# Kernel tuning notes

Measured on AMD Instinct MI355X. Metric: run time of the kernel, lower is better.

## Reference

```python
import jax, jax.numpy as jnp
import numpy as np


def setup_inputs() -> dict:
    key = jax.random.key(0)
    k1, k2 = jax.random.split(key)
    B, H, W, C = 16, 768, 1024, 4
    source = jax.random.normal(k1, (B, H, W, C), dtype=jnp.float32)
    # flow in pixels; scale so some warps land out of bounds (exercises safe path)
    flow = jax.random.normal(k2, (B, H, W, 2), dtype=jnp.float32) * 20.0
    return {"source": source, "flow": flow}


def _bilinear_resample_safe(data, warp_x, warp_y):
    """Bilinear sampling of data [B,H,W,C] at (warp_x, warp_y) [B,H,W].
    Out-of-bounds corner taps contribute 0 (TF safe_gather_nd semantics)."""
    B, H, W, C = data.shape
    fx = jnp.floor(warp_x)
    fy = jnp.floor(warp_y)
    w_right = warp_x - fx          # [B,H,W]
    w_down = warp_y - fy
    w_left = 1.0 - w_right
    w_up = 1.0 - w_down
    x0 = fx.astype(jnp.int32)
    y0 = fy.astype(jnp.int32)
    x1 = jnp.ceil(warp_x).astype(jnp.int32)
    y1 = jnp.ceil(warp_y).astype(jnp.int32)
    b = jnp.broadcast_to(jnp.arange(B, dtype=jnp.int32)[:, None, None], warp_x.shape)

    def gather(yy, xx):
        valid = (yy >= 0) & (yy <= H - 1) & (xx >= 0) & (xx <= W - 1)
        yc = jnp.clip(yy, 0, H - 1)
        xc = jnp.clip(xx, 0, W - 1)
        return data[b, yc, xc] * valid[..., None].astype(data.dtype)  # [B,H,W,C]

    wl = w_left[..., None]
    wr = w_right[..., None]
    wu = w_up[..., None]
    wd = w_down[..., None]
    return ((gather(y0, x0) * wl + gather(y0, x1) * wr) * wu
            + (gather(y1, x0) * wl + gather(y1, x1) * wr) * wd)


def reference(source, flow):
    B, H, W, _ = flow.shape
    # flow_to_warp: grid (i=y, j=x) + flow
    gy, gx = jnp.meshgrid(jnp.linspace(0.0, H - 1.0, H),
                          jnp.linspace(0.0, W - 1.0, W), indexing='ij')
    warp = jnp.stack([gy, gx], axis=-1).astype(flow.dtype) + flow  # [B,H,W,2] (y,x)
    warp_y = warp[..., 0]
    warp_x = warp[..., 1]  # resample reverses last dim: (y,x) -> (x,y) for resampler
    warped = _bilinear_resample_safe(source, warp_x, warp_y)
    # mask_invalid on warp coords
    mask = ((warp_y >= 0.0) & (warp_y <= H - 1.0)
            & (warp_x >= 0.0) & (warp_x <= W - 1.0)).astype(warped.dtype)[..., None]
    return warped * mask
```

## Files before the change

### kernel.cpp

```cpp
#include <hip/hip_runtime.h>


typedef float v2f __attribute__((ext_vector_type(2)));
typedef float v4f __attribute__((ext_vector_type(4)));

constexpr int B = 16, H = 768, W = 1024;
constexpr int TX = 64;
constexpr int TY = 16;
constexpr int RPT = 4;
constexpr int XT = W / TX;
constexpr int YT = H / TY;
constexpr int NWG = B * XT * YT;
constexpr int NXCD = 8;
constexpr int CHUNK = NWG / NXCD;

__global__ __launch_bounds__(256) void warp_bilinear_kernel(
    const float* __restrict__ src,
    const float* __restrict__ flow,
    float* __restrict__ out)
{
    unsigned orig = blockIdx.x;
    unsigned t = (orig & (NXCD - 1)) * CHUNK + (orig >> 3);

    int xt = t & (XT - 1);
    unsigned tt = t >> 4;
    int yt = (int)(tt % YT);
    int b  = (int)(tt / YT);

    int tx = threadIdx.x & 63;
    int wv = threadIdx.x >> 6;

    int x     = (xt << 6) + tx;
    int ybase = yt * TY + wv * RPT;

    const float4* sb = (const float4*)src + b * (H * W);
    const v2f*    fb = (const v2f*)flow;
    v4f*          ob = (v4f*)out;

    float xf = (float)x;

#pragma unroll
    for (int r = 0; r < RPT; ++r) {
        int y   = ybase + r;
        int pix = (b * H + y) * W + x;

        v2f fl = __builtin_nontemporal_load(fb + pix);
        float wy = (float)y + fl.x;
        float wx = xf       + fl.y;

        v4f result = {0.f, 0.f, 0.f, 0.f};

        bool valid = (wy >= 0.f) & (wy <= (float)(H - 1)) &
                     (wx >= 0.f) & (wx <= (float)(W - 1));
        if (valid) {
            float fx = floorf(wx);
            float fy = floorf(wy);
            int x0 = (int)fx;
            int y0 = (int)fy;
            int x1 = (int)ceilf(wx);
            int y1 = (int)ceilf(wy);
            float wr = wx - fx;
            float wd = wy - fy;
            float wl = 1.f - wr;
            float wu = 1.f - wd;

            const float4* row0 = sb + y0 * W;
            const float4* row1 = sb + y1 * W;
            float4 g00 = row0[x0];
            float4 g01 = row0[x1];
            float4 g10 = row1[x0];
            float4 g11 = row1[x1];

            result.x = (g00.x * wl + g01.x * wr) * wu + (g10.x * wl + g11.x * wr) * wd;
            result.y = (g00.y * wl + g01.y * wr) * wu + (g10.y * wl + g11.y * wr) * wd;
            result.z = (g00.z * wl + g01.z * wr) * wu + (g10.z * wl + g11.z * wr) * wd;
            result.w = (g00.w * wl + g01.w * wr) * wu + (g10.w * wl + g11.w * wr) * wd;
        }

        __builtin_nontemporal_store(result, ob + pix);
    }
}

extern "C" void kernel_launch(void* const* d_in, const int* in_sizes, int n_in,
                              void* d_out, int out_size, void* d_ws, size_t ws_size,
                              hipStream_t stream) {
    const float* src  = (const float*)d_in[0];
    const float* flow = (const float*)d_in[1];
    float* out = (float*)d_out;

    warp_bilinear_kernel<<<NWG, 256, 0, stream>>>(src, flow, out);
}
```

Measured before the change: 560.7 us.

## Batch flow loads and branchless clamped gathers across rows for memory-level parallelism

```diff
diff --git a/kernel.cpp b/kernel.cpp
--- a/kernel.cpp
+++ b/kernel.cpp
@@ -6,8 +6,8 @@
 
 constexpr int B = 16, H = 768, W = 1024;
 constexpr int TX = 64;
-constexpr int TY = 16;
-constexpr int RPT = 4;
+constexpr int TY = 8;
+constexpr int RPT = 2;
 constexpr int XT = W / TX;
 constexpr int YT = H / TY;
 constexpr int NWG = B * XT * YT;
@@ -33,51 +33,63 @@
     int x     = (xt << 6) + tx;
     int ybase = yt * TY + wv * RPT;
 
-    const float4* sb = (const float4*)src + b * (H * W);
-    const v2f*    fb = (const v2f*)flow;
-    v4f*          ob = (v4f*)out;
+    const v4f* sb = (const v4f*)src + b * (H * W);
+    const v2f* fb = (const v2f*)flow;
+    v4f*       ob = (v4f*)out;
 
-    float xf = (float)x;
+    float xf  = (float)x;
+    int  pix0 = (b * H + ybase) * W + x;
+
+    v2f fl[RPT];
+#pragma unroll
+    for (int r = 0; r < RPT; ++r)
+        fl[r] = __builtin_nontemporal_load(fb + pix0 + r * W);
+
+    int   o00[RPT], o01[RPT], o10[RPT], o11[RPT];
+    float wl[RPT], wr[RPT], wu[RPT], wd[RPT], vm[RPT];
+#pragma unroll
+    for (int r = 0; r < RPT; ++r) {
+        float wy = (float)(ybase + r) + fl[r].x;
+        float wx = xf                 + fl[r].y;
+
+        bool valid = (wy >= 0.f) & (wy <= (float)(H - 1)) &
+                     (wx >= 0.f) & (wx <= (float)(W - 1));
+        vm[r] = valid ? 1.f : 0.f;
+
+        float cy = fminf(fmaxf(wy, 0.f), (float)(H - 1));
+        float cx = fminf(fmaxf(wx, 0.f), (float)(W - 1));
+
+        float fx = floorf(cx);
+        float fy = floorf(cy);
+        int x0 = (int)fx;
+        int y0 = (int)fy;
+        int x1 = (int)ceilf(cx);
+        int y1 = (int)ceilf(cy);
+        wr[r] = cx - fx;
+        wd[r] = cy - fy;
+        wl[r] = 1.f - wr[r];
+        wu[r] = 1.f - wd[r];
+
+        o00[r] = y0 * W + x0;
+        o01[r] = y0 * W + x1;
+        o10[r] = y1 * W + x0;
+        o11[r] = y1 * W + x1;
+    }
+
+    v4f g00[RPT], g01[RPT], g10[RPT], g11[RPT];
+#pragma unroll
+    for (int r = 0; r < RPT; ++r) {
+        g00[r] = sb[o00[r]];
+        g01[r] = sb[o01[r]];
+        g10[r] = sb[o10[r]];
+        g11[r] = sb[o11[r]];
+    }
 
 #pragma unroll
     for (int r = 0; r < RPT; ++r) {
-        int y   = ybase + r;
-        int pix = (b * H + y) * W + x;
-
-        v2f fl = __builtin_nontemporal_load(fb + pix);
-        float wy = (float)y + fl.x;
-        float wx = xf       + fl.y;
-
-        v4f result = {0.f, 0.f, 0.f, 0.f};
-
-        bool valid = (wy >= 0.f) & (wy <= (float)(H - 1)) &
-                     (wx >= 0.f) & (wx <= (float)(W - 1));
-        if (valid) {
-            float fx = floorf(wx);
-            float fy = floorf(wy);
-            int x0 = (int)fx;
-            int y0 = (int)fy;
-            int x1 = (int)ceilf(wx);
-            int y1 = (int)ceilf(wy);
-            float wr = wx - fx;
-            float wd = wy - fy;
-            float wl = 1.f - wr;
-            float wu = 1.f - wd;
-
-            const float4* row0 = sb + y0 * W;
-            const float4* row1 = sb + y1 * W;
-            float4 g00 = row0[x0];
-            float4 g01 = row0[x1];
-            float4 g10 = row1[x0];
-            float4 g11 = row1[x1];
-
-            result.x = (g00.x * wl + g01.x * wr) * wu + (g10.x * wl + g11.x * wr) * wd;
-            result.y = (g00.y * wl + g01.y * wr) * wu + (g10.y * wl + g11.y * wr) * wd;
-            result.z = (g00.z * wl + g01.z * wr) * wu + (g10.z * wl + g11.z * wr) * wd;
-            result.w = (g00.w * wl + g01.w * wr) * wu + (g10.w * wl + g11.w * wr) * wd;
-        }
-
-        __builtin_nontemporal_store(result, ob + pix);
+        v4f res = ((g00[r] * wl[r] + g01[r] * wr[r]) * wu[r]
+                 + (g10[r] * wl[r] + g11[r] * wr[r]) * wd[r]) * vm[r];
+        __builtin_nontemporal_store(res, ob + pix0 + r * W);
     }
 }
 
```

New measurement: 575.5 us. +2.7%, slower.
